# Performance work log

Hardware: AMD Instinct MI355X
Metric: run time of the kernel (lower is better)

The kernel has to match this reference:

```python
import jax, jax.numpy as jnp
import numpy as np

B, S, C = 1, 6, 128
Hf, Wf = 56, 100            # feature map (stride-8 of 448x800)
IMG_H, IMG_W = 448, 800
Z, Y, X = 128, 8, 128
BOUNDS = (-50.0, 50.0, -5.0, 5.0, -50.0, 50.0)
CENTROID = (0.0, 0.1, 0.0)
EPS = 1e-6


def _voxel_centers():
    # ref-frame (cam0) coordinates of voxel centers, Vox_util.Mem2Ref of gridcloud3d
    xmin, xmax = BOUNDS[0] + CENTROID[0], BOUNDS[1] + CENTROID[0]
    ymin, ymax = BOUNDS[2] + CENTROID[1], BOUNDS[3] + CENTROID[1]
    zmin, zmax = BOUNDS[4] + CENTROID[2], BOUNDS[5] + CENTROID[2]
    vsx, vsy, vsz = (xmax - xmin) / X, (ymax - ymin) / Y, (zmax - zmin) / Z
    zi, yi, xi = jnp.meshgrid(jnp.arange(Z), jnp.arange(Y), jnp.arange(X), indexing='ij')
    xr = xmin + vsx * 0.5 + xi.astype(jnp.float32) * vsx
    yr = ymin + vsy * 0.5 + yi.astype(jnp.float32) * vsy
    zr = zmin + vsz * 0.5 + zi.astype(jnp.float32) * vsz
    return jnp.stack([xr.reshape(-1), yr.reshape(-1), zr.reshape(-1)], axis=-1)  # (N,3), N=Z*Y*X


def setup_inputs() -> dict:
    key = jax.random.key(0)
    k1, k2 = jax.random.split(key)
    cam_feat = jax.random.normal(k1, (B, S, C, Hf, Wf), dtype=jnp.float32)
    # intrinsics: fx=fy=500, principal point at image center
    K = np.zeros((B, S, 4, 4), np.float32)
    K[..., 0, 0] = 500.0; K[..., 1, 1] = 500.0
    K[..., 0, 2] = IMG_W / 2.0; K[..., 1, 2] = IMG_H / 2.0
    K[..., 2, 2] = 1.0; K[..., 3, 3] = 1.0
    # surround-view rig: rotate about y (camera-frame vertical) by 2*pi*s/S
    ang = np.arange(S) * (2.0 * np.pi / S)
    c, s = np.cos(ang).astype(np.float32), np.sin(ang).astype(np.float32)
    R = np.zeros((B, S, 3, 3), np.float32)
    R[..., 0, 0] = c; R[..., 0, 2] = s; R[..., 1, 1] = 1.0
    R[..., 2, 0] = -s; R[..., 2, 2] = c
    t = np.stack([0.5 * s, np.full(S, -1.0, np.float32), 0.5 * c], axis=-1)[None].astype(np.float32)
    conv_w = jax.random.normal(k2, (C, C * Y, 3, 3), dtype=jnp.float32) * 0.02
    return {
        'cam_feat': cam_feat,
        'intrins': jnp.asarray(K),
        'rots': jnp.asarray(R),
        'trans': jnp.asarray(t),
        'conv_w': conv_w,
    }


def reference(cam_feat, intrins, rots, trans, conv_w):
    Bn, Sn = cam_feat.shape[:2]
    BS = Bn * Sn
    # velo_T_cams = [R|t]; cam0_T_camXs = inv(velo_T_cams[:,0]) @ velo_T_cams
    velo_T = (jnp.zeros((Bn, Sn, 4, 4), cam_feat.dtype)
              .at[..., :3, :3].set(rots)
              .at[..., :3, 3].set(trans)
              .at[..., 3, 3].set(1.0))
    cam0_T_camXs = jnp.einsum('bij,bsjk->bsik', jnp.linalg.inv(velo_T[:, 0]), velo_T)
    camXs_T_cam0 = jnp.linalg.inv(cam0_T_camXs)  # (B,S,4,4)
    # scale_intrinsics to feature resolution
    sx, sy = Wf / float(IMG_W), Hf / float(IMG_H)
    Kf = (jnp.zeros((Bn, Sn, 4, 4), cam_feat.dtype)
          .at[..., 0, 0].set(intrins[..., 0, 0] * sx)
          .at[..., 1, 1].set(intrins[..., 1, 1] * sy)
          .at[..., 0, 2].set(intrins[..., 0, 2] * sx)
          .at[..., 1, 2].set(intrins[..., 1, 2] * sy)
          .at[..., 2, 2].set(1.0).at[..., 3, 3].set(1.0))
    pixB_T_cam0 = jnp.einsum('bsij,bsjk->bsik', Kf, camXs_T_cam0).reshape(BS, 4, 4)
    camXs_T_cam0 = camXs_T_cam0.reshape(BS, 4, 4)

    xyz = _voxel_centers()                                   # (N,3)
    xyz1 = jnp.concatenate([xyz, jnp.ones((xyz.shape[0], 1), xyz.dtype)], axis=-1)  # (N,4)
    cam_pts = jnp.einsum('pij,nj->pni', camXs_T_cam0, xyz1)  # (BS,N,4)
    z = cam_pts[..., 2]
    pix = jnp.einsum('pij,nj->pni', pixB_T_cam0, xyz1)       # (BS,N,4)
    denom = jnp.maximum(pix[..., 2:3], EPS)
    x = pix[..., 0] / denom[..., 0]
    y = pix[..., 1] / denom[..., 0]
    valid = (x > -0.5) & (x < Wf - 0.5) & (y > -0.5) & (y < Hf - 0.5) & (z > 0.0)

    # normalize_grid2d + grid_sample(align_corners=False) unnormalization
    gx = jnp.clip(2.0 * x / (Wf - 1) - 1.0, -2.0, 2.0)
    gy = jnp.clip(2.0 * y / (Hf - 1) - 1.0, -2.0, 2.0)
    ux = ((gx + 1.0) * Wf - 1.0) * 0.5
    uy = ((gy + 1.0) * Hf - 1.0) * 0.5
    x0f, y0f = jnp.floor(ux), jnp.floor(uy)
    wx, wy = ux - x0f, uy - y0f
    x0i, y0i = x0f.astype(jnp.int32), y0f.astype(jnp.int32)

    feat = cam_feat.reshape(BS, C, Hf * Wf)

    def corner(xi, yi, w):
        inb = (xi >= 0) & (xi < Wf) & (yi >= 0) & (yi < Hf)  # zeros padding
        idx = jnp.clip(yi, 0, Hf - 1) * Wf + jnp.clip(xi, 0, Wf - 1)
        v = jnp.take_along_axis(feat, idx[:, None, :], axis=2)  # (BS,C,N)
        return v * (w * inb.astype(w.dtype))[:, None, :]

    vals = (corner(x0i, y0i, (1 - wx) * (1 - wy))
            + corner(x0i + 1, y0i, wx * (1 - wy))
            + corner(x0i, y0i + 1, (1 - wx) * wy)
            + corner(x0i + 1, y0i + 1, wx * wy))
    vals = vals * valid[:, None, :].astype(vals.dtype)
    feat_mems = vals.reshape(Bn, Sn, C, Z, Y, X)

    # reduce_masked_mean over cameras
    mask = (jnp.abs(feat_mems) > 0).astype(feat_mems.dtype)
    feat_mem = jnp.sum(feat_mems * mask, axis=1) / (EPS + jnp.sum(mask, axis=1))  # (B,C,Z,Y,X)

    # BEV compress: permute(0,1,3,2,4) -> (B, C*Y, Z, X), conv3x3 + InstanceNorm + GELU
    bev = jnp.transpose(feat_mem, (0, 1, 3, 2, 4)).reshape(Bn, C * Y, Z, X)
    out = jax.lax.conv_general_dilated(bev, conv_w, (1, 1), 'SAME',
                                       dimension_numbers=('NCHW', 'OIHW', 'NCHW'))
    mu = out.mean(axis=(2, 3), keepdims=True)
    var = out.var(axis=(2, 3), keepdims=True)
    out = (out - mu) * jax.lax.rsqrt(var + 1e-5)
    return jax.nn.gelu(out, approximate=False)
```

## Files before the change

### kernel.cpp

```cpp
#include <hip/hip_runtime.h>
#include <cmath>

#define SNUM 6
#define CNUM 128
#define HF 56
#define WF 100
#define HW (HF*WF)
#define ZN 128
#define YN 8
#define XN 128
#define NVOX (ZN*YN*XN)

typedef __attribute__((ext_vector_type(8))) short bf16x8;
typedef __attribute__((ext_vector_type(4))) float f32x4;
typedef __attribute__((ext_vector_type(4))) int   i32x4;

__device__ __forceinline__ unsigned short f2bf(float f) {
    unsigned u = __builtin_bit_cast(unsigned, f);
    unsigned r = (u + 0x7FFFu + ((u >> 16) & 1u)) >> 16;
    return (unsigned short)r;
}
__device__ __forceinline__ float bf2f(unsigned short h) {
    unsigned u = (unsigned)h << 16;
    return __builtin_bit_cast(float, u);
}

__device__ __forceinline__ void gl_lds16(const void* g, void* l) {
    __builtin_amdgcn_global_load_lds(
        (const __attribute__((address_space(1))) void*)g,
        (__attribute__((address_space(3))) void*)l, 16, 0, 0);
}
__device__ __forceinline__ void gl_lds4(const void* g, void* l) {
    __builtin_amdgcn_global_load_lds(
        (const __attribute__((address_space(1))) void*)g,
        (__attribute__((address_space(3))) void*)l, 4, 0, 0);
}

__global__ void k_setup(const float* __restrict__ intrins,
                        const float* __restrict__ rots,
                        const float* __restrict__ trans,
                        float* __restrict__ mats) {
    int s = threadIdx.x;
    if (s >= SNUM) return;
    float R0[9], Rs[9], t0[3], ts[3];
    for (int i = 0; i < 9; ++i) { R0[i] = rots[i]; Rs[i] = rots[s*9 + i]; }
    for (int i = 0; i < 3; ++i) { t0[i] = trans[i]; ts[i] = trans[s*3 + i]; }
    float M[3][4];
    float d0 = t0[0]-ts[0], d1 = t0[1]-ts[1], d2 = t0[2]-ts[2];
    for (int i = 0; i < 3; ++i) {
        for (int j = 0; j < 3; ++j)
            M[i][j] = Rs[0*3+i]*R0[0*3+j] + Rs[1*3+i]*R0[1*3+j] + Rs[2*3+i]*R0[2*3+j];
        M[i][3] = Rs[0*3+i]*d0 + Rs[1*3+i]*d1 + Rs[2*3+i]*d2;
    }
    const float sx = (float)WF/800.0f, sy = (float)HF/448.0f;
    float fx = intrins[s*16 + 0]*sx, fy = intrins[s*16 + 5]*sy;
    float cx = intrins[s*16 + 2]*sx, cy = intrins[s*16 + 6]*sy;
    float* o = mats + s*24;
    for (int j = 0; j < 4; ++j) {
        o[0*4+j]      = M[0][j];
        o[1*4+j]      = M[1][j];
        o[2*4+j]      = M[2][j];
        o[12 + 0*4+j] = fx*M[0][j] + cx*M[2][j];
        o[12 + 1*4+j] = fy*M[1][j] + cy*M[2][j];
        o[12 + 2*4+j] = M[2][j];
    }
}

__global__ __launch_bounds__(256) void k_tfeat(const float* __restrict__ cf,
                                               unsigned short* __restrict__ featT) {
    __shared__ float t[32][33];
    int s = blockIdx.z;
    int p0 = blockIdx.x * 32, c0 = blockIdx.y * 32;
    int tx = threadIdx.x, ty = threadIdx.y;
#pragma unroll
    for (int k = 0; k < 4; ++k) {
        int r = ty + k*8;
        t[r][tx] = cf[((size_t)s*CNUM + c0 + r)*HW + p0 + tx];
    }
    __syncthreads();
#pragma unroll
    for (int k = 0; k < 4; ++k) {
        int r = ty + k*8;
        featT[((size_t)s*HW + p0 + r)*CNUM + c0 + tx] = f2bf(t[tx][r]);
    }
}

__global__ __launch_bounds__(256) void k_geo(const float* __restrict__ mats,
                                             float* __restrict__ uv) {
#pragma clang fp contract(off)
    int n = blockIdx.x * 256 + threadIdx.x;
    int zi = n >> 10, yi = (n >> 7) & 7, xi = n & 127;
    float xr = -49.609375f + (float)xi * 0.78125f;
    float yr = (-4.9f + 0.625f) + (float)yi * 1.25f;
    float zr = -49.609375f + (float)zi * 0.78125f;
#pragma unroll
    for (int s = 0; s < SNUM; ++s) {
        const float* m = mats + s*24;
        float zc = m[8]*xr  + m[9]*yr  + m[10]*zr + m[11];
        float ph = m[12]*xr + m[13]*yr + m[14]*zr + m[15];
        float qh = m[16]*xr + m[17]*yr + m[18]*zr + m[19];
        float denom = fmaxf(zc, 1e-6f);
        float px = ph / denom, py = qh / denom;
        bool valid = (px > -0.5f) & (px < (float)WF - 0.5f) &
                     (py > -0.5f) & (py < (float)HF - 0.5f) & (zc > 0.0f);
        float ux = -10000.0f, uy = -10000.0f;
        if (valid) {
            float gx = 2.0f*px/((float)WF - 1.0f) - 1.0f;
            float gy = 2.0f*py/((float)HF - 1.0f) - 1.0f;
            gx = fminf(fmaxf(gx, -2.0f), 2.0f);
            gy = fminf(fmaxf(gy, -2.0f), 2.0f);
            ux = ((gx + 1.0f)*(float)WF - 1.0f)*0.5f;
            uy = ((gy + 1.0f)*(float)HF - 1.0f)*0.5f;
        }
        uv[(n*SNUM + s)*2]     = ux;
        uv[(n*SNUM + s)*2 + 1] = uy;
    }
}

__global__ __launch_bounds__(256) void k_zero(unsigned short* __restrict__ bevin2) {
    int i = blockIdx.x*256 + threadIdx.x;
    if (i >= 66048) return;
    size_t unit;
    if (i < 33280) {
        int zr = i / 16640;
        int j  = i - zr*16640;
        unit = (size_t)(zr ? 129 : 0)*16640 + j;
    } else {
        int j  = i - 33280;
        int zp = 1 + (j >> 8);
        int r  = j & 255;
        int c  = r >> 1;
        int xp = (r & 1) ? 129 : 0;
        unit = ((size_t)zp*128 + c)*130 + xp;
    }
    *(i32x4*)&bevin2[unit*8] = i32x4{0,0,0,0};
}

__global__ __launch_bounds__(256) void k_sample(const unsigned short* __restrict__ featT,
                                                const float* __restrict__ uv,
                                                unsigned short* __restrict__ bevin2) {
#pragma clang fp contract(off)
    __shared__ float xch[16][132];
    const int tid = threadIdx.x;
    const int b = blockIdx.x;
    const int z = b >> 6, x0 = (b & 63) * 2;
    const int cl = tid & 15, vs = tid >> 4;
    const int y = vs >> 1, xs = vs & 1;
    const int n = z*1024 + y*128 + x0 + xs;
    const bf16x8 zz8 = {0,0,0,0,0,0,0,0};
    float sum[8], cnt[8];
#pragma unroll
    for (int k = 0; k < 8; ++k) { sum[k] = 0.0f; cnt[k] = 0.0f; }
    for (int s = 0; s < SNUM; ++s) {
        float2 u = ((const float2*)uv)[n*SNUM + s];
        if (u.x < -999.0f) continue;
        float x0f = floorf(u.x), y0f = floorf(u.y);
        float wx = u.x - x0f, wy = u.y - y0f;
        int ix = (int)x0f, iy = (int)y0f;
        float w00 = (1.0f-wx)*(1.0f-wy), w10 = wx*(1.0f-wy);
        float w01 = (1.0f-wx)*wy,        w11 = wx*wy;
        bool bx0 = (ix >= 0) & (ix < WF);
        bool bx1 = (ix >= -1) & (ix < WF-1);
        bool by0 = (iy >= 0) & (iy < HF);
        bool by1 = (iy >= -1) & (iy < HF-1);
        bool c00 = bx0 & by0, c10 = bx1 & by0, c01 = bx0 & by1, c11 = bx1 & by1;
        const unsigned short* fb = featT + (size_t)s * (HW*CNUM) + cl*8;
        long r0 = (long)(iy*WF + ix) * CNUM;
        bf16x8 v00 = c00 ? *(const bf16x8*)(fb + r0)                 : zz8;
        bf16x8 v10 = c10 ? *(const bf16x8*)(fb + r0 + CNUM)          : zz8;
        bf16x8 v01 = c01 ? *(const bf16x8*)(fb + r0 + WF*CNUM)       : zz8;
        bf16x8 v11 = c11 ? *(const bf16x8*)(fb + r0 + WF*CNUM + CNUM): zz8;
#pragma unroll
        for (int k = 0; k < 8; ++k) {
            float v = 0.0f;
            v = v + w00 * bf2f((unsigned short)v00[k]);
            v = v + w10 * bf2f((unsigned short)v10[k]);
            v = v + w01 * bf2f((unsigned short)v01[k]);
            v = v + w11 * bf2f((unsigned short)v11[k]);
            sum[k] += v;
            cnt[k] += (v != 0.0f) ? 1.0f : 0.0f;
        }
    }
#pragma unroll
    for (int k = 0; k < 8; ++k)
        xch[vs][cl*8 + k] = sum[k] / (1e-6f + cnt[k]);
    __syncthreads();
    {
        int c = tid >> 1, xs2 = tid & 1;
        unsigned pk[4];
#pragma unroll
        for (int j = 0; j < 4; ++j) {
            float v0 = xch[(2*j)*2 + xs2][c];
            float v1 = xch[(2*j+1)*2 + xs2][c];
            pk[j] = (unsigned)f2bf(v0) | ((unsigned)f2bf(v1) << 16);
        }
        size_t unit = ((size_t)(z+1)*128 + c)*130 + (x0 + xs2 + 1);
        *(i32x4*)&bevin2[unit*8] = i32x4{(int)pk[0], (int)pk[1], (int)pk[2], (int)pk[3]};
    }
}

__global__ __launch_bounds__(256) void k_wprep(const float* __restrict__ w,
                                               unsigned short* __restrict__ w2) {
    int i = blockIdx.x*256 + threadIdx.x;
    if (i >= 9*128*1024) return;
    int ci = i & 1023; int rest = i >> 10; int co = rest & 127; int tap = rest >> 7;
    w2[i] = f2bf(w[((size_t)co*1024 + ci)*9 + tap]);
}

__global__ __launch_bounds__(128, 1) void k_conv_mfma(
        const unsigned short* __restrict__ bevin2,
        const unsigned short* __restrict__ w2,
        float* __restrict__ out) {
    __shared__ __align__(16) unsigned short lds[2][12*80*8];
    const int tid  = threadIdx.x;
    const int z0   = blockIdx.x;
    const int coh  = blockIdx.y >> 1;
    const int xh   = blockIdx.y & 1;
    const int lane = tid & 63, wr = tid >> 6;
    const int co_base = coh*64 + wr*32;
    const int l15 = lane & 15, lhi = lane >> 4;

    f32x4 acc[2][4];
#pragma unroll
    for (int f = 0; f < 2; ++f)
#pragma unroll
        for (int nf = 0; nf < 4; ++nf) acc[f][nf] = f32x4{0.f,0.f,0.f,0.f};

    const unsigned short* aw0 = w2 + ((size_t)(co_base      + l15))*1024 + lhi*8;
    const unsigned short* aw1 = w2 + ((size_t)(co_base + 16 + l15))*1024 + lhi*8;

    bf16x8 afr0[18], afr1[18];

#define STAGE(BUF, C0)                                                         \
    {                                                                          \
        _Pragma("unroll")                                                      \
        for (int r6 = 0; r6 < 6; ++r6) {                                       \
            int r = wr*6 + r6;                                                 \
            int dzr = r >> 2, cg = r & 3;                                      \
            const unsigned short* gsrc = bevin2 +                              \
                (((size_t)(z0 + dzr)*128 + (C0) + cg)*130 + xh*64)*8;          \
            unsigned short* ldst = &lds[BUF][r*80*8];                          \
            gl_lds16(gsrc + (size_t)lane*8, ldst);                             \
            gl_lds4 (gsrc + 64*8 + (size_t)lane*2, ldst + 64*8);               \
        }                                                                      \
    }
#define A_LOAD(DST, CI0)                                                       \
    {                                                                          \
        _Pragma("unroll")                                                      \
        for (int t = 0; t < 9; ++t) {                                          \
            DST[t*2]   = *(const bf16x8*)(aw0 + (size_t)t*131072 + (CI0));     \
            DST[t*2+1] = *(const bf16x8*)(aw1 + (size_t)t*131072 + (CI0));     \
        }                                                                      \
    }
#define COMPUTE(BUF, AFR)                                                      \
    {                                                                          \
        __builtin_amdgcn_s_setprio(1);                                         \
        _Pragma("unroll")                                                      \
        for (int dz = 0; dz < 3; ++dz) {                                       \
            _Pragma("unroll")                                                  \
            for (int dx = 0; dx < 3; ++dx) {                                   \
                bf16x8 a0 = AFR[(dz*3+dx)*2];                                  \
                bf16x8 a1 = AFR[(dz*3+dx)*2+1];                                \
                _Pragma("unroll")                                              \
                for (int nf = 0; nf < 4; ++nf) {                               \
                    bf16x8 bfr = *(const bf16x8*)&lds[BUF][((dz*4 + lhi)*80 + nf*16 + l15 + dx)*8]; \
                    acc[0][nf] = __builtin_amdgcn_mfma_f32_16x16x32_bf16(a0, bfr, acc[0][nf], 0, 0, 0); \
                    acc[1][nf] = __builtin_amdgcn_mfma_f32_16x16x32_bf16(a1, bfr, acc[1][nf], 0, 0, 0); \
                }                                                              \
            }                                                                  \
        }                                                                      \
        __builtin_amdgcn_s_setprio(0);                                         \
    }

    STAGE(0, 0);
    A_LOAD(afr0, 0);
    __syncthreads();

    for (int cc = 0; cc < 16; ++cc) {
        const int k0 = 2*cc;
        STAGE(1, (k0+1)*4);
        A_LOAD(afr1, (k0+1)*32);
        COMPUTE(0, afr0);
        __syncthreads();
        if (cc < 15) {
            STAGE(0, (k0+2)*4);
            A_LOAD(afr0, (k0+2)*32);
        }
        COMPUTE(1, afr1);
        if (cc < 15) __syncthreads();
    }

#pragma unroll
    for (int f = 0; f < 2; ++f)
#pragma unroll
        for (int nf = 0; nf < 4; ++nf)
#pragma unroll
            for (int r = 0; r < 4; ++r) {
                int co = co_base + f*16 + lhi*4 + r;
                out[(size_t)co*16384 + z0*128 + xh*64 + nf*16 + l15] = acc[f][nf][r];
            }
#undef STAGE
#undef A_LOAD
#undef COMPUTE
}

__global__ __launch_bounds__(256) void k_instnorm_stats(const float* __restrict__ out,
                                                        float* __restrict__ stats) {
    __shared__ float r1[256], r2[256];
    int co = blockIdx.x, tid = threadIdx.x;
    const float* p = out + (size_t)co*16384;
    float s1 = 0.0f, s2 = 0.0f;
    for (int i = tid; i < 16384; i += 256) { float v = p[i]; s1 += v; s2 += v*v; }
    r1[tid] = s1; r2[tid] = s2;
    __syncthreads();
    for (int off = 128; off > 0; off >>= 1) {
        if (tid < off) { r1[tid] += r1[tid+off]; r2[tid] += r2[tid+off]; }
        __syncthreads();
    }
    if (tid == 0) {
        float mean = r1[0] * (1.0f/16384.0f);
        float var  = r2[0] * (1.0f/16384.0f) - mean*mean;
        stats[co*2]   = mean;
        stats[co*2+1] = rsqrtf(var + 1e-5f);
    }
}

__global__ __launch_bounds__(256) void k_gelu(float* __restrict__ out,
                                              const float* __restrict__ stats) {
    int i = blockIdx.x*256 + threadIdx.x;
    int co = i >> 14;
    float v = out[i];
    float r = (v - stats[co*2]) * stats[co*2+1];
    out[i] = 0.5f * r * (1.0f + erff(r * 0.70710678118654752f));
}

extern "C" void kernel_launch(void* const* d_in, const int* in_sizes, int n_in,
                              void* d_out, int out_size, void* d_ws, size_t ws_size,
                              hipStream_t stream) {
    const float* cam_feat = (const float*)d_in[0];
    const float* intrins  = (const float*)d_in[1];
    const float* rots     = (const float*)d_in[2];
    const float* trans    = (const float*)d_in[3];
    const float* conv_w   = (const float*)d_in[4];
    float* out = (float*)d_out;
    float* ws  = (float*)d_ws;

    float* mats  = ws;
    float* uv    = ws + 160;
    unsigned short* featT  = (unsigned short*)(uv + (size_t)NVOX*12);
    unsigned short* bevin2 = featT + (size_t)SNUM*HW*CNUM;
    unsigned short* w2     = bevin2 + (size_t)130*128*130*8;
    float* stats = (float*)(w2 + 9*128*1024);

    hipLaunchKernelGGL(k_setup, dim3(1), dim3(64), 0, stream, intrins, rots, trans, mats);
    hipLaunchKernelGGL(k_tfeat, dim3(HW/32, CNUM/32, SNUM), dim3(32,8), 0, stream, cam_feat, featT);
    hipLaunchKernelGGL(k_geo, dim3(NVOX/256), dim3(256), 0, stream, mats, uv);
    hipLaunchKernelGGL(k_wprep, dim3((9*128*1024 + 255)/256), dim3(256), 0, stream, conv_w, w2);
    hipLaunchKernelGGL(k_zero, dim3((66048 + 255)/256), dim3(256), 0, stream, bevin2);
    hipLaunchKernelGGL(k_sample, dim3(8192), dim3(256), 0, stream, featT, uv, bevin2);
    hipLaunchKernelGGL(k_conv_mfma, dim3(128, 4), dim3(128), 0, stream, bevin2, w2, out);
    hipLaunchKernelGGL(k_instnorm_stats, dim3(128), dim3(256), 0, stream, out, stats);
    hipLaunchKernelGGL(k_gelu, dim3(8192), dim3(256), 0, stream, out, stats);
}
```

Measured before the change: 155.7 us.

## Fuse projection into sampling, split conv K across waves, fuse norm partial stats

Voxel projection is now computed per block inside the sampling kernel and kept in shared memory, which removes the separate geometry kernel and its uv buffer round trip. The conv kernel now runs 256 threads per block, and two wave groups each handle half of the input channels. Their partial accumulators are reduced through LDS, which doubles the waves available to hide latency. The conv epilogue also produces per-block sum and sum-of-squares partials, so the stats kernel no longer rereads the full conv output. This costs extra LDS, an added reduction step, and register pressure under launch_bounds(256,2).

```diff
diff --git a/kernel.cpp b/kernel.cpp
--- a/kernel.cpp
+++ b/kernel.cpp
@@ -85,16 +85,42 @@
     }
 }
 
-__global__ __launch_bounds__(256) void k_geo(const float* __restrict__ mats,
-                                             float* __restrict__ uv) {
+__global__ __launch_bounds__(256) void k_zero(unsigned short* __restrict__ bevin2) {
+    int i = blockIdx.x*256 + threadIdx.x;
+    if (i >= 66048) return;
+    size_t unit;
+    if (i < 33280) {
+        int zr = i / 16640;
+        int j  = i - zr*16640;
+        unit = (size_t)(zr ? 129 : 0)*16640 + j;
+    } else {
+        int j  = i - 33280;
+        int zp = 1 + (j >> 8);
+        int r  = j & 255;
+        int c  = r >> 1;
+        int xp = (r & 1) ? 129 : 0;
+        unit = ((size_t)zp*128 + c)*130 + xp;
+    }
+    *(i32x4*)&bevin2[unit*8] = i32x4{0,0,0,0};
+}
+
+__global__ __launch_bounds__(256) void k_sample(const unsigned short* __restrict__ featT,
+                                                const float* __restrict__ mats,
+                                                unsigned short* __restrict__ bevin2) {
 #pragma clang fp contract(off)
-    int n = blockIdx.x * 256 + threadIdx.x;
-    int zi = n >> 10, yi = (n >> 7) & 7, xi = n & 127;
-    float xr = -49.609375f + (float)xi * 0.78125f;
-    float yr = (-4.9f + 0.625f) + (float)yi * 1.25f;
-    float zr = -49.609375f + (float)zi * 0.78125f;
-#pragma unroll
-    for (int s = 0; s < SNUM; ++s) {
+    __shared__ float xch[16][132];
+    __shared__ float2 suv[16][6];
+    const int tid = threadIdx.x;
+    const int b = blockIdx.x;
+    const int z = b >> 6, x0 = (b & 63) * 2;
+    const int cl = tid & 15, vs = tid >> 4;
+    const int y = vs >> 1, xs = vs & 1;
+    if (tid < 96) {
+        int v = tid / 6, s = tid - (tid/6)*6;
+        int yi = v >> 1, xi2 = x0 + (v & 1);
+        float xr = -49.609375f + (float)xi2 * 0.78125f;
+        float yr = (-4.9f + 0.625f) + (float)yi * 1.25f;
+        float zr = -49.609375f + (float)z * 0.78125f;
         const float* m = mats + s*24;
         float zc = m[8]*xr  + m[9]*yr  + m[10]*zr + m[11];
         float ph = m[12]*xr + m[13]*yr + m[14]*zr + m[15];
@@ -112,47 +138,16 @@
             ux = ((gx + 1.0f)*(float)WF - 1.0f)*0.5f;
             uy = ((gy + 1.0f)*(float)HF - 1.0f)*0.5f;
         }
-        uv[(n*SNUM + s)*2]     = ux;
-        uv[(n*SNUM + s)*2 + 1] = uy;
-    }
-}
-
-__global__ __launch_bounds__(256) void k_zero(unsigned short* __restrict__ bevin2) {
-    int i = blockIdx.x*256 + threadIdx.x;
-    if (i >= 66048) return;
-    size_t unit;
-    if (i < 33280) {
-        int zr = i / 16640;
-        int j  = i - zr*16640;
-        unit = (size_t)(zr ? 129 : 0)*16640 + j;
-    } else {
-        int j  = i - 33280;
-        int zp = 1 + (j >> 8);
-        int r  = j & 255;
-        int c  = r >> 1;
-        int xp = (r & 1) ? 129 : 0;
-        unit = ((size_t)zp*128 + c)*130 + xp;
-    }
-    *(i32x4*)&bevin2[unit*8] = i32x4{0,0,0,0};
-}
-
-__global__ __launch_bounds__(256) void k_sample(const unsigned short* __restrict__ featT,
-                                                const float* __restrict__ uv,
-                                                unsigned short* __restrict__ bevin2) {
-#pragma clang fp contract(off)
-    __shared__ float xch[16][132];
-    const int tid = threadIdx.x;
-    const int b = blockIdx.x;
-    const int z = b >> 6, x0 = (b & 63) * 2;
-    const int cl = tid & 15, vs = tid >> 4;
-    const int y = vs >> 1, xs = vs & 1;
-    const int n = z*1024 + y*128 + x0 + xs;
+        suv[v][s] = float2{ux, uy};
+    }
+    __syncthreads();
+
     const bf16x8 zz8 = {0,0,0,0,0,0,0,0};
     float sum[8], cnt[8];
 #pragma unroll
     for (int k = 0; k < 8; ++k) { sum[k] = 0.0f; cnt[k] = 0.0f; }
     for (int s = 0; s < SNUM; ++s) {
-        float2 u = ((const float2*)uv)[n*SNUM + s];
+        float2 u = suv[vs][s];
         if (u.x < -999.0f) continue;
         float x0f = floorf(u.x), y0f = floorf(u.y);
         float wx = u.x - x0f, wy = u.y - y0f;
@@ -207,16 +202,18 @@
     w2[i] = f2bf(w[((size_t)co*1024 + ci)*9 + tap]);
 }
 
-__global__ __launch_bounds__(128, 1) void k_conv_mfma(
+__global__ __launch_bounds__(256, 2) void k_conv_mfma(
         const unsigned short* __restrict__ bevin2,
         const unsigned short* __restrict__ w2,
-        float* __restrict__ out) {
-    __shared__ __align__(16) unsigned short lds[2][12*80*8];
+        float* __restrict__ out,
+        float* __restrict__ psum, float* __restrict__ psq) {
+    __shared__ __align__(16) unsigned short lds[2][2][12*80*8];
     const int tid  = threadIdx.x;
     const int z0   = blockIdx.x;
     const int coh  = blockIdx.y >> 1;
     const int xh   = blockIdx.y & 1;
-    const int lane = tid & 63, wr = tid >> 6;
+    const int lane = tid & 63, wid = tid >> 6;
+    const int wr = wid & 1, kh = wid >> 1;
     const int co_base = coh*64 + wr*32;
     const int l15 = lane & 15, lhi = lane >> 4;
 
@@ -226,20 +223,20 @@
 #pragma unroll
         for (int nf = 0; nf < 4; ++nf) acc[f][nf] = f32x4{0.f,0.f,0.f,0.f};
 
-    const unsigned short* aw0 = w2 + ((size_t)(co_base      + l15))*1024 + lhi*8;
-    const unsigned short* aw1 = w2 + ((size_t)(co_base + 16 + l15))*1024 + lhi*8;
+    const unsigned short* aw0 = w2 + ((size_t)(co_base      + l15))*1024 + kh*512 + lhi*8;
+    const unsigned short* aw1 = w2 + ((size_t)(co_base + 16 + l15))*1024 + kh*512 + lhi*8;
 
     bf16x8 afr0[18], afr1[18];
 
-#define STAGE(BUF, C0)                                                         \
+#define STAGE(BUF, STEP)                                                       \
     {                                                                          \
         _Pragma("unroll")                                                      \
         for (int r6 = 0; r6 < 6; ++r6) {                                       \
             int r = wr*6 + r6;                                                 \
             int dzr = r >> 2, cg = r & 3;                                      \
             const unsigned short* gsrc = bevin2 +                              \
-                (((size_t)(z0 + dzr)*128 + (C0) + cg)*130 + xh*64)*8;          \
-            unsigned short* ldst = &lds[BUF][r*80*8];                          \
+                (((size_t)(z0 + dzr)*128 + kh*64 + (STEP)*4 + cg)*130 + xh*64)*8; \
+            unsigned short* ldst = &lds[kh][BUF][r*80*8];                      \
             gl_lds16(gsrc + (size_t)lane*8, ldst);                             \
             gl_lds4 (gsrc + 64*8 + (size_t)lane*2, ldst + 64*8);               \
         }                                                                      \
@@ -263,7 +260,7 @@
                 bf16x8 a1 = AFR[(dz*3+dx)*2+1];                                \
                 _Pragma("unroll")                                              \
                 for (int nf = 0; nf < 4; ++nf) {                               \
-                    bf16x8 bfr = *(const bf16x8*)&lds[BUF][((dz*4 + lhi)*80 + nf*16 + l15 + dx)*8]; \
+                    bf16x8 bfr = *(const bf16x8*)&lds[kh][BUF][((dz*4 + lhi)*80 + nf*16 + l15 + dx)*8]; \
                     acc[0][nf] = __builtin_amdgcn_mfma_f32_16x16x32_bf16(a0, bfr, acc[0][nf], 0, 0, 0); \
                     acc[1][nf] = __builtin_amdgcn_mfma_f32_16x16x32_bf16(a1, bfr, acc[1][nf], 0, 0, 0); \
                 }                                                              \
@@ -276,42 +273,80 @@
     A_LOAD(afr0, 0);
     __syncthreads();
 
-    for (int cc = 0; cc < 16; ++cc) {
-        const int k0 = 2*cc;
-        STAGE(1, (k0+1)*4);
-        A_LOAD(afr1, (k0+1)*32);
+    for (int ss = 0; ss < 8; ++ss) {
+        const int s0 = 2*ss;
+        STAGE(1, s0 + 1);
+        A_LOAD(afr1, (s0 + 1)*32);
         COMPUTE(0, afr0);
         __syncthreads();
-        if (cc < 15) {
-            STAGE(0, (k0+2)*4);
-            A_LOAD(afr0, (k0+2)*32);
+        if (ss < 7) {
+            STAGE(0, s0 + 2);
+            A_LOAD(afr0, (s0 + 2)*32);
         }
         COMPUTE(1, afr1);
-        if (cc < 15) __syncthreads();
-    }
-
-#pragma unroll
-    for (int f = 0; f < 2; ++f)
-#pragma unroll
-        for (int nf = 0; nf < 4; ++nf)
+        if (ss < 7) __syncthreads();
+    }
+
+    __syncthreads();
+    float* lds_f = (float*)&lds[0][0][0];
+    if (kh == 1) {
+#pragma unroll
+        for (int f = 0; f < 2; ++f)
+#pragma unroll
+            for (int nf = 0; nf < 4; ++nf)
+#pragma unroll
+                for (int r = 0; r < 4; ++r)
+                    lds_f[wr*2048 + (f*16 + lhi*4 + r)*64 + nf*16 + l15] = acc[f][nf][r];
+    }
+    __syncthreads();
+    if (kh == 0) {
+        float ps[2][4], pq[2][4];
+#pragma unroll
+        for (int f = 0; f < 2; ++f)
+#pragma unroll
+            for (int r = 0; r < 4; ++r) { ps[f][r] = 0.0f; pq[f][r] = 0.0f; }
+#pragma unroll
+        for (int f = 0; f < 2; ++f)
+#pragma unroll
+            for (int nf = 0; nf < 4; ++nf)
+#pragma unroll
+                for (int r = 0; r < 4; ++r) {
+                    int co = co_base + f*16 + lhi*4 + r;
+                    float v = acc[f][nf][r] + lds_f[wr*2048 + (f*16 + lhi*4 + r)*64 + nf*16 + l15];
+                    out[(size_t)co*16384 + z0*128 + xh*64 + nf*16 + l15] = v;
+                    ps[f][r] += v;
+                    pq[f][r] += v*v;
+                }
+#pragma unroll
+        for (int f = 0; f < 2; ++f)
 #pragma unroll
             for (int r = 0; r < 4; ++r) {
-                int co = co_base + f*16 + lhi*4 + r;
-                out[(size_t)co*16384 + z0*128 + xh*64 + nf*16 + l15] = acc[f][nf][r];
+                float s = ps[f][r], q = pq[f][r];
+#pragma unroll
+                for (int m = 1; m < 16; m <<= 1) {
+                    s += __shfl_xor(s, m);
+                    q += __shfl_xor(q, m);
+                }
+                if (l15 == 0) {
+                    int co = co_base + f*16 + lhi*4 + r;
+                    int pb = z0*2 + xh;
+                    psum[co*256 + pb] = s;
+                    psq [co*256 + pb] = q;
+                }
             }
+    }
 #undef STAGE
 #undef A_LOAD
 #undef COMPUTE
 }
 
-__global__ __launch_bounds__(256) void k_instnorm_stats(const float* __restrict__ out,
-                                                        float* __restrict__ stats) {
+__global__ __launch_bounds__(256) void k_stats(const float* __restrict__ psum,
+                                               const float* __restrict__ psq,
+                                               float* __restrict__ stats) {
     __shared__ float r1[256], r2[256];
     int co = blockIdx.x, tid = threadIdx.x;
-    const float* p = out + (size_t)co*16384;
-    float s1 = 0.0f, s2 = 0.0f;
-    for (int i = tid; i < 16384; i += 256) { float v = p[i]; s1 += v; s2 += v*v; }
-    r1[tid] = s1; r2[tid] = s2;
+    r1[tid] = psum[co*256 + tid];
+    r2[tid] = psq [co*256 + tid];
     __syncthreads();
     for (int off = 128; off > 0; off >>= 1) {
         if (tid < off) { r1[tid] += r1[tid+off]; r2[tid] += r2[tid+off]; }
@@ -346,19 +381,19 @@
     float* ws  = (float*)d_ws;
 
     float* mats  = ws;
-    float* uv    = ws + 160;
-    unsigned short* featT  = (unsigned short*)(uv + (size_t)NVOX*12);
+    unsigned short* featT  = (unsigned short*)(ws + 160);
     unsigned short* bevin2 = featT + (size_t)SNUM*HW*CNUM;
     unsigned short* w2     = bevin2 + (size_t)130*128*130*8;
-    float* stats = (float*)(w2 + 9*128*1024);
+    float* psum  = (float*)(w2 + 9*128*1024);
+    float* psq   = psum + 32768;
+    float* stats = psq + 32768;
 
     hipLaunchKernelGGL(k_setup, dim3(1), dim3(64), 0, stream, intrins, rots, trans, mats);
     hipLaunchKernelGGL(k_tfeat, dim3(HW/32, CNUM/32, SNUM), dim3(32,8), 0, stream, cam_feat, featT);
-    hipLaunchKernelGGL(k_geo, dim3(NVOX/256), dim3(256), 0, stream, mats, uv);
     hipLaunchKernelGGL(k_wprep, dim3((9*128*1024 + 255)/256), dim3(256), 0, stream, conv_w, w2);
     hipLaunchKernelGGL(k_zero, dim3((66048 + 255)/256), dim3(256), 0, stream, bevin2);
-    hipLaunchKernelGGL(k_sample, dim3(8192), dim3(256), 0, stream, featT, uv, bevin2);
-    hipLaunchKernelGGL(k_conv_mfma, dim3(128, 4), dim3(128), 0, stream, bevin2, w2, out);
-    hipLaunchKernelGGL(k_instnorm_stats, dim3(128), dim3(256), 0, stream, out, stats);
+    hipLaunchKernelGGL(k_sample, dim3(8192), dim3(256), 0, stream, featT, mats, bevin2);
+    hipLaunchKernelGGL(k_conv_mfma, dim3(128, 4), dim3(256), 0, stream, bevin2, w2, out, psum, psq);
+    hipLaunchKernelGGL(k_stats, dim3(128), dim3(256), 0, stream, psum, psq, stats);
     hipLaunchKernelGGL(k_gelu, dim3(8192), dim3(256), 0, stream, out, stats);
 }
```

Measured after the change: 175.3 us. 12.6% more time.
